# Optimization experiments

Hardware: AMD Instinct MI355X
Metric: run time of the kernel (lower is better)

## Reference

```python
import jax, jax.numpy as jnp
import numpy as np

BSZ, KW, D_MODEL, TEXT_DIM, VOCAB = 128, 8, 768, 512, 49408
EPS = 1e-8  # matches torch F.cosine_similarity eps


def setup_inputs() -> dict:
    key = jax.random.key(0)
    k1, k2, k3, k4 = jax.random.split(key, 4)
    return {
        "keywords": jax.random.normal(k1, (BSZ, KW, D_MODEL), dtype=jnp.float32),
        "W_proj": jax.random.normal(k2, (D_MODEL, TEXT_DIM), dtype=jnp.float32) * (1.0 / np.sqrt(D_MODEL)),
        "b_proj": jax.random.normal(k3, (TEXT_DIM,), dtype=jnp.float32) * 0.02,
        "W_emb": jax.random.normal(k4, (VOCAB, TEXT_DIM), dtype=jnp.float32) * 0.02,
    }


def reference(keywords, W_proj, b_proj, W_emb):
    # linear_proj: [B, K, d_model] -> [B, K, text_dim]
    kw = jnp.einsum("bkm,md->bkd", keywords, W_proj) + b_proj
    # cosine similarity of each keyword against the full token-embedding table
    kw_n = kw / jnp.maximum(jnp.linalg.norm(kw, axis=-1, keepdims=True), EPS)
    emb_n = W_emb / jnp.maximum(jnp.linalg.norm(W_emb, axis=-1, keepdims=True), EPS)
    cos_score = jnp.einsum("bkd,vd->bkv", kw_n, emb_n)  # [B, K, V]
    # soft VQ: subword probability over vocab
    subword_prob = jax.nn.softmax(cos_score, axis=-1)
    # soft assignment against the (frozen) embedding table
    kw_out = jnp.einsum("bkv,vd->bkd", subword_prob, W_emb)  # [B, K, text_dim]
    return kw_out, subword_prob, cos_score
```

## Files before the change

kernel.cpp:

```cpp
#include <hip/hip_runtime.h>

#define VOC 49408
#define TD 512
#define DM 768
#define NCOLG2 193
#define PV_S 32

typedef __attribute__((ext_vector_type(8))) short bf16x8;
typedef __attribute__((ext_vector_type(4))) short bf16x4;
typedef __attribute__((ext_vector_type(4))) float f32x4;

__device__ __forceinline__ unsigned short f2bf(float f) {
  unsigned int u = __float_as_uint(f);
  u += 0x7fffu + ((u >> 16) & 1u);
  return (unsigned short)(u >> 16);
}

__device__ __forceinline__ void gload16(const void* g, const void* l) {
  __builtin_amdgcn_global_load_lds(
      (const __attribute__((address_space(1))) void*)g,
      (__attribute__((address_space(3))) void*)l, 16, 0, 0);
}

__global__ __launch_bounds__(256) void k_proj(const float* __restrict__ kw,
                                              const float* __restrict__ Wp,
                                              const float* __restrict__ bp,
                                              unsigned short* __restrict__ kwn) {
  __shared__ float row_lds[4 * DM];
  __shared__ float rsum[4][4];
  __shared__ float rinv_s[4];
  const int t = threadIdx.x;
  const int rb = blockIdx.x * 4;
  for (int i = 0; i < 12; ++i) {
    int idx = i * 256 + t;
    row_lds[idx] = kw[(size_t)rb * DM + idx];
  }
  __syncthreads();
  float acc[4][2] = {};
  for (int m = 0; m < DM; ++m) {
    float w0 = Wp[m * TD + t];
    float w1 = Wp[m * TD + t + 256];
#pragma unroll
    for (int r = 0; r < 4; ++r) {
      float kv = row_lds[r * DM + m];
      acc[r][0] = fmaf(kv, w0, acc[r][0]);
      acc[r][1] = fmaf(kv, w1, acc[r][1]);
    }
  }
  const float b0 = bp[t], b1 = bp[t + 256];
  float p[4];
#pragma unroll
  for (int r = 0; r < 4; ++r) {
    acc[r][0] += b0;
    acc[r][1] += b1;
    p[r] = acc[r][0] * acc[r][0] + acc[r][1] * acc[r][1];
  }
#pragma unroll
  for (int off = 32; off; off >>= 1) {
#pragma unroll
    for (int r = 0; r < 4; ++r) p[r] += __shfl_down(p[r], off);
  }
  const int lane = t & 63, wv = t >> 6;
  if (lane == 0) {
#pragma unroll
    for (int r = 0; r < 4; ++r) rsum[r][wv] = p[r];
  }
  __syncthreads();
  if (t < 4) {
    float s = rsum[t][0] + rsum[t][1] + rsum[t][2] + rsum[t][3];
    rinv_s[t] = 1.0f / fmaxf(sqrtf(s), 1e-8f);
  }
  __syncthreads();
#pragma unroll
  for (int r = 0; r < 4; ++r) {
    float ri = rinv_s[r];
    kwn[(size_t)(rb + r) * TD + t] = f2bf(acc[r][0] * ri);
    kwn[(size_t)(rb + r) * TD + t + 256] = f2bf(acc[r][1] * ri);
  }
}

__global__ __launch_bounds__(256) void k_norms(const float* __restrict__ We,
                                               unsigned short* __restrict__ embB,
                                               float* __restrict__ rnormv) {
  const int t = threadIdx.x;
  const int lane = t & 63, w = t >> 6;
  const int v = blockIdx.x * 4 + w;
  const float* rowp = We + (size_t)v * TD;
  float4 a = *(const float4*)(rowp + lane * 8);
  float4 b = *(const float4*)(rowp + lane * 8 + 4);
  bf16x8 o;
  o[0] = (short)f2bf(a.x); o[1] = (short)f2bf(a.y);
  o[2] = (short)f2bf(a.z); o[3] = (short)f2bf(a.w);
  o[4] = (short)f2bf(b.x); o[5] = (short)f2bf(b.y);
  o[6] = (short)f2bf(b.z); o[7] = (short)f2bf(b.w);
  *(bf16x8*)(embB + (size_t)v * TD + lane * 8) = o;
  float ss = a.x * a.x + a.y * a.y + a.z * a.z + a.w * a.w +
             b.x * b.x + b.y * b.y + b.z * b.z + b.w * b.w;
#pragma unroll
  for (int off = 1; off < 64; off <<= 1) ss += __shfl_xor(ss, off);
  if (lane == 0) rnormv[v] = 1.0f / fmaxf(sqrtf(ss), 1e-8f);
}

__global__ __launch_bounds__(256) void k_transpose(const unsigned short* __restrict__ embB,
                                                   unsigned short* __restrict__ embT) {
  __shared__ unsigned short tile[64 * 72];
  const int t = threadIdx.x;
  const int d0 = blockIdx.x * 64, v0 = blockIdx.y * 64;
#pragma unroll
  for (int p = 0; p < 2; ++p) {
    int vl = p * 32 + (t >> 3), ch = t & 7;
    *(bf16x8*)&tile[vl * 72 + ch * 8] =
        *(const bf16x8*)(embB + (size_t)(v0 + vl) * TD + d0 + ch * 8);
  }
  __syncthreads();
#pragma unroll
  for (int p = 0; p < 2; ++p) {
    int dl = p * 32 + (t >> 3), vch = t & 7;
    bf16x8 o;
#pragma unroll
    for (int i = 0; i < 8; ++i) o[i] = (short)tile[(vch * 8 + i) * 72 + dl];
    *(bf16x8*)(embT + (size_t)(d0 + dl) * VOC + v0 + vch * 8) = o;
  }
}

__global__ __launch_bounds__(512, 2) void k_cos(const unsigned short* __restrict__ kwn,
                                                const unsigned short* __restrict__ embB,
                                                const float* __restrict__ rnormv,
                                                float* __restrict__ cosd,
                                                float* __restrict__ partial) {
  __shared__ unsigned short smem[2][2][256 * 64];
  const int t = threadIdx.x;
  const int lane = t & 63, w = t >> 6;
  const int wr = w & 3, wc = w >> 2;
  const int g = lane >> 4, l15 = lane & 15;
  const int rowg = blockIdx.x;
  const int colg = blockIdx.y;

  const int rl = lane >> 3;
  const int bsl = (lane & 7) ^ rl;

  f32x4 acc[4][8];
#pragma unroll
  for (int mi = 0; mi < 4; ++mi)
#pragma unroll
    for (int ni = 0; ni < 8; ++ni)
#pragma unroll
      for (int j = 0; j < 4; ++j) acc[mi][ni][j] = 0.0f;

  const unsigned short* Ag = kwn + (size_t)(rowg * 256 + w * 8 + rl) * TD + bsl * 8;
  const unsigned short* Bg = embB + (size_t)(colg * 256 + w * 8 + rl) * TD + bsl * 8;

#pragma unroll
  for (int i = 0; i < 4; ++i) {
    gload16(Ag + (size_t)(i * 64) * TD, (const void*)(&smem[0][0][(i * 64 + w * 8) * 64]));
    gload16(Bg + (size_t)(i * 64) * TD, (const void*)(&smem[0][1][(i * 64 + w * 8) * 64]));
  }
  __syncthreads();

  for (int kt = 0; kt < 8; ++kt) {
    const int buf = kt & 1;
    if (kt < 7) {
#pragma unroll
      for (int i = 0; i < 4; ++i) {
        gload16(Ag + (size_t)(i * 64) * TD + (kt + 1) * 64,
                (const void*)(&smem[buf ^ 1][0][(i * 64 + w * 8) * 64]));
        gload16(Bg + (size_t)(i * 64) * TD + (kt + 1) * 64,
                (const void*)(&smem[buf ^ 1][1][(i * 64 + w * 8) * 64]));
      }
    }
#pragma unroll
    for (int ks = 0; ks < 2; ++ks) {
      const int ch = (((ks * 4 + g) ^ (l15 & 7)) << 3);
      bf16x8 a[4];
#pragma unroll
      for (int mi = 0; mi < 4; ++mi)
        a[mi] = *(const bf16x8*)&smem[buf][0][(wr * 64 + mi * 16 + l15) * 64 + ch];
#pragma unroll
      for (int ni = 0; ni < 8; ++ni) {
        bf16x8 b = *(const bf16x8*)&smem[buf][1][(wc * 128 + ni * 16 + l15) * 64 + ch];
#pragma unroll
        for (int mi = 0; mi < 4; ++mi)
          acc[mi][ni] = __builtin_amdgcn_mfma_f32_16x16x32_bf16(a[mi], b, acc[mi][ni], 0, 0, 0);
      }
    }
    __syncthreads();
  }

  float (*rs)[256] = (float(*)[256]) & smem[0][0][0];
  const size_t rowbase = (size_t)rowg * 256 + wr * 64;
  const int colbase = colg * 256 + wc * 128;
  float rnv[8];
#pragma unroll
  for (int ni = 0; ni < 8; ++ni) rnv[ni] = rnormv[colbase + ni * 16 + l15];
#pragma unroll
  for (int mi = 0; mi < 4; ++mi) {
    float es[4] = {0.f, 0.f, 0.f, 0.f};
#pragma unroll
    for (int ni = 0; ni < 8; ++ni) {
#pragma unroll
      for (int j = 0; j < 4; ++j) {
        float c = acc[mi][ni][j] * rnv[ni];
        cosd[(rowbase + mi * 16 + g * 4 + j) * VOC + colbase + ni * 16 + l15] = c;
        es[j] += __expf(c);
      }
    }
#pragma unroll
    for (int j = 0; j < 4; ++j) {
      float e = es[j];
      e += __shfl_xor(e, 1);
      e += __shfl_xor(e, 2);
      e += __shfl_xor(e, 4);
      e += __shfl_xor(e, 8);
      if (l15 == 0) rs[wc][wr * 64 + mi * 16 + g * 4 + j] = e;
    }
  }
  __syncthreads();
  if (t < 256) {
    float srow = rs[0][t] + rs[1][t];
    partial[(size_t)colg * 1024 + rowg * 256 + t] = srow;
  }
}

__global__ __launch_bounds__(256) void k_denom(const float* __restrict__ partial,
                                               float* __restrict__ rdenom) {
  const int t = threadIdx.x;
  const int lane = t & 63, w = t >> 6;
  const int row = blockIdx.x * 4 + w;
  float s = 0.f;
  for (int c = lane; c < NCOLG2; c += 64) s += partial[(size_t)c * 1024 + row];
#pragma unroll
  for (int off = 1; off < 64; off <<= 1) s += __shfl_xor(s, off);
  if (lane == 0) rdenom[row] = 1.0f / s;
}

__global__ __launch_bounds__(512, 2) void k_pv(const float* __restrict__ cosd,
                                               const unsigned short* __restrict__ embT,
                                               const float* __restrict__ rdenom,
                                               float* __restrict__ prob,
                                               float* __restrict__ kpart) {
  __shared__ unsigned short smem[2][2][256 * 64];
  const int t = threadIdx.x;
  const int lane = t & 63, w = t >> 6;
  const int wr = w & 3, wc = w >> 2;
  const int g = lane >> 4, l15 = lane & 15;
  const int rowg = blockIdx.x;
  const int colg = blockIdx.y;
  const int s = blockIdx.z;
  const int t0 = s * 24 + (s < 4 ? s : 4);
  const int t1 = t0 + 24 + (s < 4 ? 1 : 0);

  const int ar = t >> 1, ah = t & 1;
  const int grow = rowg * 256 + ar;
  const float rdv = rdenom[grow];
  const float* cbase = cosd + (size_t)grow * VOC + ah * 4;
  float* pbase = prob + (size_t)grow * VOC + ah * 4;

  const int rl = lane >> 3;
  const int bsl = (lane & 7) ^ rl;

  f32x4 acc[4][8];
#pragma unroll
  for (int mi = 0; mi < 4; ++mi)
#pragma unroll
    for (int ni = 0; ni < 8; ++ni)
#pragma unroll
      for (int j = 0; j < 4; ++j) acc[mi][ni][j] = 0.0f;

  float4 cc[8];
  {
    const float* cp = cbase + (size_t)t0 * 64;
#pragma unroll
    for (int i = 0; i < 8; ++i) cc[i] = *(const float4*)(cp + i * 8);
  }

#pragma unroll
  for (int i = 0; i < 4; ++i) {
    gload16(embT + (size_t)(colg * 256 + i * 64 + w * 8 + rl) * VOC + t0 * 64 + bsl * 8,
            (const void*)(&smem[0][1][(i * 64 + w * 8) * 64]));
  }
  {
    const bool wp = (colg == (t0 & 1));
#pragma unroll
    for (int i = 0; i < 8; ++i) {
      float4 px;
      px.x = __expf(cc[i].x) * rdv;
      px.y = __expf(cc[i].y) * rdv;
      px.z = __expf(cc[i].z) * rdv;
      px.w = __expf(cc[i].w) * rdv;
      if (wp) *(float4*)(pbase + (size_t)t0 * 64 + i * 8) = px;
      bf16x4 b4;
      b4[0] = (short)f2bf(px.x);
      b4[1] = (short)f2bf(px.y);
      b4[2] = (short)f2bf(px.z);
      b4[3] = (short)f2bf(px.w);
      *(bf16x4*)&smem[0][0][ar * 64 + ((i ^ (ar & 7)) << 3) + ah * 4] = b4;
    }
  }
  if (t0 + 1 < t1) {
    const float* cp = cbase + (size_t)(t0 + 1) * 64;
#pragma unroll
    for (int i = 0; i < 8; ++i) cc[i] = *(const float4*)(cp + i * 8);
  }
  __syncthreads();

  for (int kt = t0; kt < t1; ++kt) {
    const int buf = (kt - t0) & 1;
    if (kt + 1 < t1) {
#pragma unroll
      for (int i = 0; i < 4; ++i) {
        gload16(embT + (size_t)(colg * 256 + i * 64 + w * 8 + rl) * VOC + (kt + 1) * 64 + bsl * 8,
                (const void*)(&smem[buf ^ 1][1][(i * 64 + w * 8) * 64]));
      }
      const bool wp = (colg == ((kt + 1) & 1));
#pragma unroll
      for (int i = 0; i < 8; ++i) {
        float4 px;
        px.x = __expf(cc[i].x) * rdv;
        px.y = __expf(cc[i].y) * rdv;
        px.z = __expf(cc[i].z) * rdv;
        px.w = __expf(cc[i].w) * rdv;
        if (wp) *(float4*)(pbase + (size_t)(kt + 1) * 64 + i * 8) = px;
        bf16x4 b4;
        b4[0] = (short)f2bf(px.x);
        b4[1] = (short)f2bf(px.y);
        b4[2] = (short)f2bf(px.z);
        b4[3] = (short)f2bf(px.w);
        *(bf16x4*)&smem[buf ^ 1][0][ar * 64 + ((i ^ (ar & 7)) << 3) + ah * 4] = b4;
      }
      if (kt + 2 < t1) {
        const float* cp = cbase + (size_t)(kt + 2) * 64;
#pragma unroll
        for (int i = 0; i < 8; ++i) cc[i] = *(const float4*)(cp + i * 8);
      }
    }
#pragma unroll
    for (int ks = 0; ks < 2; ++ks) {
      const int ch = (((ks * 4 + g) ^ (l15 & 7)) << 3);
      bf16x8 a[4];
#pragma unroll
      for (int mi = 0; mi < 4; ++mi)
        a[mi] = *(const bf16x8*)&smem[buf][0][(wr * 64 + mi * 16 + l15) * 64 + ch];
#pragma unroll
      for (int ni = 0; ni < 8; ++ni) {
        bf16x8 b = *(const bf16x8*)&smem[buf][1][(wc * 128 + ni * 16 + l15) * 64 + ch];
#pragma unroll
        for (int mi = 0; mi < 4; ++mi)
          acc[mi][ni] = __builtin_amdgcn_mfma_f32_16x16x32_bf16(a[mi], b, acc[mi][ni], 0, 0, 0);
      }
    }
    __syncthreads();
  }

#pragma unroll
  for (int mi = 0; mi < 4; ++mi)
#pragma unroll
    for (int ni = 0; ni < 8; ++ni)
#pragma unroll
      for (int j = 0; j < 4; ++j)
        kpart[((size_t)s * 1024 + rowg * 256 + wr * 64 + mi * 16 + g * 4 + j) * TD +
              colg * 256 + wc * 128 + ni * 16 + l15] = acc[mi][ni][j];
}

__global__ __launch_bounds__(256) void k_kwout(const float* __restrict__ kpart,
                                               float* __restrict__ outp) {
  const int gid = blockIdx.x * 256 + threadIdx.x;
  float4 s = {0.f, 0.f, 0.f, 0.f};
#pragma unroll
  for (int sp = 0; sp < PV_S; ++sp) {
    float4 v = *(const float4*)(kpart + (size_t)sp * 524288 + gid * 4);
    s.x += v.x; s.y += v.y; s.z += v.z; s.w += v.w;
  }
  *(float4*)(outp + gid * 4) = s;
}

extern "C" void kernel_launch(void* const* d_in, const int* in_sizes, int n_in,
                              void* d_out, int out_size, void* d_ws, size_t ws_size,
                              hipStream_t stream) {
  const float* kw = (const float*)d_in[0];
  const float* Wp = (const float*)d_in[1];
  const float* bp = (const float*)d_in[2];
  const float* We = (const float*)d_in[3];
  float* out = (float*)d_out;
  char* ws = (char*)d_ws;

  unsigned short* embT = (unsigned short*)ws;
  unsigned short* embB = (unsigned short*)(ws + 50593792);
  unsigned short* kwn = (unsigned short*)(ws + 101187584);
  float* rnormv = (float*)(ws + 102236160);
  float* partial = (float*)(ws + 102433792);
  float* rdenom = (float*)(ws + 103224320);
  float* kpart = (float*)(ws + 103228416);

  float* kwout = out;
  float* prob = out + 524288;
  float* cosd = out + 51118080;

  hipLaunchKernelGGL(k_proj, dim3(256), dim3(256), 0, stream, kw, Wp, bp, kwn);
  hipLaunchKernelGGL(k_norms, dim3(12352), dim3(256), 0, stream, We, embB, rnormv);
  hipLaunchKernelGGL(k_transpose, dim3(8, 772), dim3(256), 0, stream, embB, embT);
  hipLaunchKernelGGL(k_cos, dim3(4, NCOLG2), dim3(512), 0, stream, kwn, embB, rnormv,
                     cosd, partial);
  hipLaunchKernelGGL(k_denom, dim3(256), dim3(256), 0, stream, partial, rdenom);
  hipLaunchKernelGGL(k_pv, dim3(4, 2, PV_S), dim3(512), 0, stream, cosd, embT, rdenom,
                     prob, kpart);
  hipLaunchKernelGGL(k_kwout, dim3(512), dim3(256), 0, stream, kpart, kwout);
}
```

Before: 377.7 us.

## Store bf16 exp scores in cos kernel and feed them directly to PV

The cosine kernel now also writes exp(cos) as bf16 into a workspace buffer, staged through LDS for coalesced stores. The PV kernel loads that buffer with async global-to-LDS copies instead of rereading fp32 cos scores and recomputing exp. The 1/denominator scaling moves out of the MFMA operand into the final k_kwout reduction, and the prob output is written from the LDS tile. This halves the bytes read for the A operand and drops per-element exp work in PV, at the cost of an extra bf16 write of the full score matrix in k_cos and prob values rounded from bf16 exp.

Result: no change. 381.1 us (+0.9%).

```diff
diff --git a/kernel.cpp b/kernel.cpp
--- a/kernel.cpp
+++ b/kernel.cpp
@@ -14,6 +14,10 @@
   unsigned int u = __float_as_uint(f);
   u += 0x7fffu + ((u >> 16) & 1u);
   return (unsigned short)(u >> 16);
+}
+
+__device__ __forceinline__ float bf2f(unsigned short h) {
+  return __uint_as_float(((unsigned int)h) << 16);
 }
 
 __device__ __forceinline__ void gload16(const void* g, const void* l) {
@@ -127,8 +131,10 @@
                                                 const unsigned short* __restrict__ embB,
                                                 const float* __restrict__ rnormv,
                                                 float* __restrict__ cosd,
+                                                unsigned short* __restrict__ eb,
                                                 float* __restrict__ partial) {
   __shared__ unsigned short smem[2][2][256 * 64];
+  __shared__ float rs[2][256];
   const int t = threadIdx.x;
   const int lane = t & 63, w = t >> 6;
   const int wr = w & 3, wc = w >> 2;
@@ -186,7 +192,7 @@
     __syncthreads();
   }
 
-  float (*rs)[256] = (float(*)[256]) & smem[0][0][0];
+  unsigned short* els = &smem[0][0][0];
   const size_t rowbase = (size_t)rowg * 256 + wr * 64;
   const int colbase = colg * 256 + wc * 128;
   float rnv[8];
@@ -201,7 +207,9 @@
       for (int j = 0; j < 4; ++j) {
         float c = acc[mi][ni][j] * rnv[ni];
         cosd[(rowbase + mi * 16 + g * 4 + j) * VOC + colbase + ni * 16 + l15] = c;
-        es[j] += __expf(c);
+        float ev = __expf(c);
+        es[j] += ev;
+        els[(wr * 64 + mi * 16 + g * 4 + j) * 256 + wc * 128 + ni * 16 + l15] = f2bf(ev);
       }
     }
 #pragma unroll
@@ -215,6 +223,13 @@
     }
   }
   __syncthreads();
+#pragma unroll
+  for (int k = 0; k < 16; ++k) {
+    int id = k * 512 + t;
+    int r = id >> 5, c8 = id & 31;
+    *(bf16x8*)(eb + (size_t)(rowg * 256 + r) * VOC + colg * 256 + c8 * 8) =
+        *(const bf16x8*)&els[r * 256 + c8 * 8];
+  }
   if (t < 256) {
     float srow = rs[0][t] + rs[1][t];
     partial[(size_t)colg * 1024 + rowg * 256 + t] = srow;
@@ -233,7 +248,7 @@
   if (lane == 0) rdenom[row] = 1.0f / s;
 }
 
-__global__ __launch_bounds__(512, 2) void k_pv(const float* __restrict__ cosd,
+__global__ __launch_bounds__(512, 2) void k_pv(const unsigned short* __restrict__ eb,
                                                const unsigned short* __restrict__ embT,
                                                const float* __restrict__ rdenom,
                                                float* __restrict__ prob,
@@ -249,14 +264,13 @@
   const int t0 = s * 24 + (s < 4 ? s : 4);
   const int t1 = t0 + 24 + (s < 4 ? 1 : 0);
 
+  const int rl = lane >> 3;
+  const int bsl = (lane & 7) ^ rl;
+
   const int ar = t >> 1, ah = t & 1;
   const int grow = rowg * 256 + ar;
   const float rdv = rdenom[grow];
-  const float* cbase = cosd + (size_t)grow * VOC + ah * 4;
-  float* pbase = prob + (size_t)grow * VOC + ah * 4;
-
-  const int rl = lane >> 3;
-  const int bsl = (lane & 7) ^ rl;
+  float* pbase = prob + (size_t)grow * VOC;
 
   f32x4 acc[4][8];
 #pragma unroll
@@ -266,40 +280,13 @@
 #pragma unroll
       for (int j = 0; j < 4; ++j) acc[mi][ni][j] = 0.0f;
 
-  float4 cc[8];
-  {
-    const float* cp = cbase + (size_t)t0 * 64;
-#pragma unroll
-    for (int i = 0; i < 8; ++i) cc[i] = *(const float4*)(cp + i * 8);
-  }
+  const unsigned short* Ag = eb + (size_t)(rowg * 256 + w * 8 + rl) * VOC + bsl * 8;
+  const unsigned short* Bg = embT + (size_t)(colg * 256 + w * 8 + rl) * VOC + bsl * 8;
 
 #pragma unroll
   for (int i = 0; i < 4; ++i) {
-    gload16(embT + (size_t)(colg * 256 + i * 64 + w * 8 + rl) * VOC + t0 * 64 + bsl * 8,
-            (const void*)(&smem[0][1][(i * 64 + w * 8) * 64]));
-  }
-  {
-    const bool wp = (colg == (t0 & 1));
-#pragma unroll
-    for (int i = 0; i < 8; ++i) {
-      float4 px;
-      px.x = __expf(cc[i].x) * rdv;
-      px.y = __expf(cc[i].y) * rdv;
-      px.z = __expf(cc[i].z) * rdv;
-      px.w = __expf(cc[i].w) * rdv;
-      if (wp) *(float4*)(pbase + (size_t)t0 * 64 + i * 8) = px;
-      bf16x4 b4;
-      b4[0] = (short)f2bf(px.x);
-      b4[1] = (short)f2bf(px.y);
-      b4[2] = (short)f2bf(px.z);
-      b4[3] = (short)f2bf(px.w);
-      *(bf16x4*)&smem[0][0][ar * 64 + ((i ^ (ar & 7)) << 3) + ah * 4] = b4;
-    }
-  }
-  if (t0 + 1 < t1) {
-    const float* cp = cbase + (size_t)(t0 + 1) * 64;
-#pragma unroll
-    for (int i = 0; i < 8; ++i) cc[i] = *(const float4*)(cp + i * 8);
+    gload16(Ag + (size_t)(i * 64) * VOC + t0 * 64, (const void*)(&smem[0][0][(i * 64 + w * 8) * 64]));
+    gload16(Bg + (size_t)(i * 64) * VOC + t0 * 64, (const void*)(&smem[0][1][(i * 64 + w * 8) * 64]));
   }
   __syncthreads();
 
@@ -308,29 +295,10 @@
     if (kt + 1 < t1) {
 #pragma unroll
       for (int i = 0; i < 4; ++i) {
-        gload16(embT + (size_t)(colg * 256 + i * 64 + w * 8 + rl) * VOC + (kt + 1) * 64 + bsl * 8,
+        gload16(Ag + (size_t)(i * 64) * VOC + (kt + 1) * 64,
+                (const void*)(&smem[buf ^ 1][0][(i * 64 + w * 8) * 64]));
+        gload16(Bg + (size_t)(i * 64) * VOC + (kt + 1) * 64,
                 (const void*)(&smem[buf ^ 1][1][(i * 64 + w * 8) * 64]));
-      }
-      const bool wp = (colg == ((kt + 1) & 1));
-#pragma unroll
-      for (int i = 0; i < 8; ++i) {
-        float4 px;
-        px.x = __expf(cc[i].x) * rdv;
-        px.y = __expf(cc[i].y) * rdv;
-        px.z = __expf(cc[i].z) * rdv;
-        px.w = __expf(cc[i].w) * rdv;
-        if (wp) *(float4*)(pbase + (size_t)(kt + 1) * 64 + i * 8) = px;
-        bf16x4 b4;
-        b4[0] = (short)f2bf(px.x);
-        b4[1] = (short)f2bf(px.y);
-        b4[2] = (short)f2bf(px.z);
-        b4[3] = (short)f2bf(px.w);
-        *(bf16x4*)&smem[buf ^ 1][0][ar * 64 + ((i ^ (ar & 7)) << 3) + ah * 4] = b4;
-      }
-      if (kt + 2 < t1) {
-        const float* cp = cbase + (size_t)(kt + 2) * 64;
-#pragma unroll
-        for (int i = 0; i < 8; ++i) cc[i] = *(const float4*)(cp + i * 8);
       }
     }
 #pragma unroll
@@ -348,6 +316,24 @@
           acc[mi][ni] = __builtin_amdgcn_mfma_f32_16x16x32_bf16(a[mi], b, acc[mi][ni], 0, 0, 0);
       }
     }
+    if (colg == (kt & 1)) {
+#pragma unroll
+      for (int i = 0; i < 4; ++i) {
+        const int c8 = 2 * i + ah;
+        bf16x8 ev = *(const bf16x8*)&smem[buf][0][ar * 64 + ((c8 ^ (ar & 7)) << 3)];
+        float4 o0, o1;
+        o0.x = bf2f((unsigned short)ev[0]) * rdv;
+        o0.y = bf2f((unsigned short)ev[1]) * rdv;
+        o0.z = bf2f((unsigned short)ev[2]) * rdv;
+        o0.w = bf2f((unsigned short)ev[3]) * rdv;
+        o1.x = bf2f((unsigned short)ev[4]) * rdv;
+        o1.y = bf2f((unsigned short)ev[5]) * rdv;
+        o1.z = bf2f((unsigned short)ev[6]) * rdv;
+        o1.w = bf2f((unsigned short)ev[7]) * rdv;
+        *(float4*)(pbase + (size_t)kt * 64 + c8 * 8) = o0;
+        *(float4*)(pbase + (size_t)kt * 64 + c8 * 8 + 4) = o1;
+      }
+    }
     __syncthreads();
   }
 
@@ -362,15 +348,20 @@
 }
 
 __global__ __launch_bounds__(256) void k_kwout(const float* __restrict__ kpart,
+                                               const float* __restrict__ rdenom,
                                                float* __restrict__ outp) {
   const int gid = blockIdx.x * 256 + threadIdx.x;
+  const int row = gid >> 7;
   float4 s = {0.f, 0.f, 0.f, 0.f};
 #pragma unroll
   for (int sp = 0; sp < PV_S; ++sp) {
     float4 v = *(const float4*)(kpart + (size_t)sp * 524288 + gid * 4);
     s.x += v.x; s.y += v.y; s.z += v.z; s.w += v.w;
   }
-  *(float4*)(outp + gid * 4) = s;
+  const float rdv = rdenom[row];
+  float4 o;
+  o.x = s.x * rdv; o.y = s.y * rdv; o.z = s.z * rdv; o.w = s.w * rdv;
+  *(float4*)(outp + gid * 4) = o;
 }
 
 extern "C" void kernel_launch(void* const* d_in, const int* in_sizes, int n_in,
@@ -389,7 +380,8 @@
   float* rnormv = (float*)(ws + 102236160);
   float* partial = (float*)(ws + 102433792);
   float* rdenom = (float*)(ws + 103224320);
-  float* kpart = (float*)(ws + 103228416);
+  unsigned short* eb = (unsigned short*)(ws + 103228416);
+  float* kpart = (float*)(ws + 204416000);
 
   float* kwout = out;
   float* prob = out + 524288;
@@ -399,9 +391,9 @@
   hipLaunchKernelGGL(k_norms, dim3(12352), dim3(256), 0, stream, We, embB, rnormv);
   hipLaunchKernelGGL(k_transpose, dim3(8, 772), dim3(256), 0, stream, embB, embT);
   hipLaunchKernelGGL(k_cos, dim3(4, NCOLG2), dim3(512), 0, stream, kwn, embB, rnormv,
-                     cosd, partial);
+                     cosd, eb, partial);
   hipLaunchKernelGGL(k_denom, dim3(256), dim3(256), 0, stream, partial, rdenom);
-  hipLaunchKernelGGL(k_pv, dim3(4, 2, PV_S), dim3(512), 0, stream, cosd, embT, rdenom,
+  hipLaunchKernelGGL(k_pv, dim3(4, 2, PV_S), dim3(512), 0, stream, eb, embT, rdenom,
                      prob, kpart);
-  hipLaunchKernelGGL(k_kwout, dim3(512), dim3(256), 0, stream, kpart, kwout);
-}
+  hipLaunchKernelGGL(k_kwout, dim3(512), dim3(256), 0, stream, kpart, rdenom, kwout);
+}
```

## Retile PV kernel to full-width 128x512 tiles so softmax is computed once

Applied to the files above, without the earlier changes.

The PV kernel used 256x256 output tiles split over two column groups, so every cosine score was read and exponentiated twice, once per column group. It now uses 128-row by 512-column tiles with K-steps of 32, so each block covers the full text dimension and every prob element is computed and stored exactly once. This halves the cosd reads and the exp work, at the cost of smaller K steps with more barriers per unit of work and reloading embT once per row group. The k_cos row-sum scratch is also moved into its own shared array instead of aliasing the tile buffer.

Result: slower. 408.9 us (+8.2%).

```diff
diff --git a/kernel.cpp b/kernel.cpp
--- a/kernel.cpp
+++ b/kernel.cpp
@@ -129,6 +129,7 @@
                                                 float* __restrict__ cosd,
                                                 float* __restrict__ partial) {
   __shared__ unsigned short smem[2][2][256 * 64];
+  __shared__ float rs[2][256];
   const int t = threadIdx.x;
   const int lane = t & 63, w = t >> 6;
   const int wr = w & 3, wc = w >> 2;
@@ -186,7 +187,6 @@
     __syncthreads();
   }
 
-  float (*rs)[256] = (float(*)[256]) & smem[0][0][0];
   const size_t rowbase = (size_t)rowg * 256 + wr * 64;
   const int colbase = colg * 256 + wc * 128;
   float rnv[8];
@@ -238,25 +238,26 @@
                                                const float* __restrict__ rdenom,
                                                float* __restrict__ prob,
                                                float* __restrict__ kpart) {
-  __shared__ unsigned short smem[2][2][256 * 64];
+  __shared__ unsigned short As[2][128 * 32];
+  __shared__ unsigned short Bs[2][512 * 32];
   const int t = threadIdx.x;
   const int lane = t & 63, w = t >> 6;
-  const int wr = w & 3, wc = w >> 2;
+  const int wr = w & 1, wc = w >> 1;
   const int g = lane >> 4, l15 = lane & 15;
   const int rowg = blockIdx.x;
-  const int colg = blockIdx.y;
-  const int s = blockIdx.z;
-  const int t0 = s * 24 + (s < 4 ? s : 4);
-  const int t1 = t0 + 24 + (s < 4 ? 1 : 0);
-
-  const int ar = t >> 1, ah = t & 1;
-  const int grow = rowg * 256 + ar;
+  const int s = blockIdx.y;
+  const int t0 = s * 48 + (s < 8 ? s : 8);
+  const int t1 = t0 + 48 + (s < 8 ? 1 : 0);
+
+  const int ar = t >> 2, q = t & 3;
+  const int grow = rowg * 128 + ar;
   const float rdv = rdenom[grow];
-  const float* cbase = cosd + (size_t)grow * VOC + ah * 4;
-  float* pbase = prob + (size_t)grow * VOC + ah * 4;
-
-  const int rl = lane >> 3;
-  const int bsl = (lane & 7) ^ rl;
+  const float* cbase = cosd + (size_t)grow * VOC + q * 8;
+  float* pbase = prob + (size_t)grow * VOC + q * 8;
+  const int aoff = ar * 32 + ((q ^ (ar & 3)) << 3);
+
+  const int rl4 = lane >> 2;
+  const int bsl = (lane & 3) ^ (rl4 & 3);
 
   f32x4 acc[4][8];
 #pragma unroll
@@ -266,40 +267,37 @@
 #pragma unroll
       for (int j = 0; j < 4; ++j) acc[mi][ni][j] = 0.0f;
 
-  float4 cc[8];
+  float4 c0, c1;
   {
-    const float* cp = cbase + (size_t)t0 * 64;
-#pragma unroll
-    for (int i = 0; i < 8; ++i) cc[i] = *(const float4*)(cp + i * 8);
+    const float* cp = cbase + (size_t)t0 * 32;
+    c0 = *(const float4*)cp;
+    c1 = *(const float4*)(cp + 4);
   }
 
 #pragma unroll
   for (int i = 0; i < 4; ++i) {
-    gload16(embT + (size_t)(colg * 256 + i * 64 + w * 8 + rl) * VOC + t0 * 64 + bsl * 8,
-            (const void*)(&smem[0][1][(i * 64 + w * 8) * 64]));
+    gload16(embT + (size_t)(w * 64 + i * 16 + rl4) * VOC + t0 * 32 + bsl * 8,
+            (const void*)(&Bs[0][(w * 64 + i * 16) * 32]));
   }
   {
-    const bool wp = (colg == (t0 & 1));
-#pragma unroll
-    for (int i = 0; i < 8; ++i) {
-      float4 px;
-      px.x = __expf(cc[i].x) * rdv;
-      px.y = __expf(cc[i].y) * rdv;
-      px.z = __expf(cc[i].z) * rdv;
-      px.w = __expf(cc[i].w) * rdv;
-      if (wp) *(float4*)(pbase + (size_t)t0 * 64 + i * 8) = px;
-      bf16x4 b4;
-      b4[0] = (short)f2bf(px.x);
-      b4[1] = (short)f2bf(px.y);
-      b4[2] = (short)f2bf(px.z);
-      b4[3] = (short)f2bf(px.w);
-      *(bf16x4*)&smem[0][0][ar * 64 + ((i ^ (ar & 7)) << 3) + ah * 4] = b4;
-    }
+    float4 p0, p1;
+    p0.x = __expf(c0.x) * rdv; p0.y = __expf(c0.y) * rdv;
+    p0.z = __expf(c0.z) * rdv; p0.w = __expf(c0.w) * rdv;
+    p1.x = __expf(c1.x) * rdv; p1.y = __expf(c1.y) * rdv;
+    p1.z = __expf(c1.z) * rdv; p1.w = __expf(c1.w) * rdv;
+    *(float4*)(pbase + (size_t)t0 * 32) = p0;
+    *(float4*)(pbase + (size_t)t0 * 32 + 4) = p1;
+    bf16x8 a8;
+    a8[0] = (short)f2bf(p0.x); a8[1] = (short)f2bf(p0.y);
+    a8[2] = (short)f2bf(p0.z); a8[3] = (short)f2bf(p0.w);
+    a8[4] = (short)f2bf(p1.x); a8[5] = (short)f2bf(p1.y);
+    a8[6] = (short)f2bf(p1.z); a8[7] = (short)f2bf(p1.w);
+    *(bf16x8*)&As[0][aoff] = a8;
   }
   if (t0 + 1 < t1) {
-    const float* cp = cbase + (size_t)(t0 + 1) * 64;
-#pragma unroll
-    for (int i = 0; i < 8; ++i) cc[i] = *(const float4*)(cp + i * 8);
+    const float* cp = cbase + (size_t)(t0 + 1) * 32;
+    c0 = *(const float4*)cp;
+    c1 = *(const float4*)(cp + 4);
   }
   __syncthreads();
 
@@ -308,41 +306,37 @@
     if (kt + 1 < t1) {
 #pragma unroll
       for (int i = 0; i < 4; ++i) {
-        gload16(embT + (size_t)(colg * 256 + i * 64 + w * 8 + rl) * VOC + (kt + 1) * 64 + bsl * 8,
-                (const void*)(&smem[buf ^ 1][1][(i * 64 + w * 8) * 64]));
-      }
-      const bool wp = (colg == ((kt + 1) & 1));
-#pragma unroll
-      for (int i = 0; i < 8; ++i) {
-        float4 px;
-        px.x = __expf(cc[i].x) * rdv;
-        px.y = __expf(cc[i].y) * rdv;
-        px.z = __expf(cc[i].z) * rdv;
-        px.w = __expf(cc[i].w) * rdv;
-        if (wp) *(float4*)(pbase + (size_t)(kt + 1) * 64 + i * 8) = px;
-        bf16x4 b4;
-        b4[0] = (short)f2bf(px.x);
-        b4[1] = (short)f2bf(px.y);
-        b4[2] = (short)f2bf(px.z);
-        b4[3] = (short)f2bf(px.w);
-        *(bf16x4*)&smem[buf ^ 1][0][ar * 64 + ((i ^ (ar & 7)) << 3) + ah * 4] = b4;
-      }
+        gload16(embT + (size_t)(w * 64 + i * 16 + rl4) * VOC + (kt + 1) * 32 + bsl * 8,
+                (const void*)(&Bs[buf ^ 1][(w * 64 + i * 16) * 32]));
+      }
+      float4 p0, p1;
+      p0.x = __expf(c0.x) * rdv; p0.y = __expf(c0.y) * rdv;
+      p0.z = __expf(c0.z) * rdv; p0.w = __expf(c0.w) * rdv;
+      p1.x = __expf(c1.x) * rdv; p1.y = __expf(c1.y) * rdv;
+      p1.z = __expf(c1.z) * rdv; p1.w = __expf(c1.w) * rdv;
+      *(float4*)(pbase + (size_t)(kt + 1) * 32) = p0;
+      *(float4*)(pbase + (size_t)(kt + 1) * 32 + 4) = p1;
+      bf16x8 a8;
+      a8[0] = (short)f2bf(p0.x); a8[1] = (short)f2bf(p0.y);
+      a8[2] = (short)f2bf(p0.z); a8[3] = (short)f2bf(p0.w);
+      a8[4] = (short)f2bf(p1.x); a8[5] = (short)f2bf(p1.y);
+      a8[6] = (short)f2bf(p1.z); a8[7] = (short)f2bf(p1.w);
+      *(bf16x8*)&As[buf ^ 1][aoff] = a8;
       if (kt + 2 < t1) {
-        const float* cp = cbase + (size_t)(kt + 2) * 64;
-#pragma unroll
-        for (int i = 0; i < 8; ++i) cc[i] = *(const float4*)(cp + i * 8);
-      }
-    }
-#pragma unroll
-    for (int ks = 0; ks < 2; ++ks) {
-      const int ch = (((ks * 4 + g) ^ (l15 & 7)) << 3);
+        const float* cp = cbase + (size_t)(kt + 2) * 32;
+        c0 = *(const float4*)cp;
+        c1 = *(const float4*)(cp + 4);
+      }
+    }
+    {
+      const int ch = ((g ^ (l15 & 3)) << 3);
       bf16x8 a[4];
 #pragma unroll
       for (int mi = 0; mi < 4; ++mi)
-        a[mi] = *(const bf16x8*)&smem[buf][0][(wr * 64 + mi * 16 + l15) * 64 + ch];
+        a[mi] = *(const bf16x8*)&As[buf][(wr * 64 + mi * 16 + l15) * 32 + ch];
 #pragma unroll
       for (int ni = 0; ni < 8; ++ni) {
-        bf16x8 b = *(const bf16x8*)&smem[buf][1][(wc * 128 + ni * 16 + l15) * 64 + ch];
+        bf16x8 b = *(const bf16x8*)&Bs[buf][(wc * 128 + ni * 16 + l15) * 32 + ch];
 #pragma unroll
         for (int mi = 0; mi < 4; ++mi)
           acc[mi][ni] = __builtin_amdgcn_mfma_f32_16x16x32_bf16(a[mi], b, acc[mi][ni], 0, 0, 0);
@@ -357,8 +351,8 @@
     for (int ni = 0; ni < 8; ++ni)
 #pragma unroll
       for (int j = 0; j < 4; ++j)
-        kpart[((size_t)s * 1024 + rowg * 256 + wr * 64 + mi * 16 + g * 4 + j) * TD +
-              colg * 256 + wc * 128 + ni * 16 + l15] = acc[mi][ni][j];
+        kpart[((size_t)s * 1024 + rowg * 128 + wr * 64 + mi * 16 + g * 4 + j) * TD +
+              wc * 128 + ni * 16 + l15] = acc[mi][ni][j];
 }
 
 __global__ __launch_bounds__(256) void k_kwout(const float* __restrict__ kpart,
@@ -401,7 +395,7 @@
   hipLaunchKernelGGL(k_cos, dim3(4, NCOLG2), dim3(512), 0, stream, kwn, embB, rnormv,
                      cosd, partial);
   hipLaunchKernelGGL(k_denom, dim3(256), dim3(256), 0, stream, partial, rdenom);
-  hipLaunchKernelGGL(k_pv, dim3(4, 2, PV_S), dim3(512), 0, stream, cosd, embT, rdenom,
+  hipLaunchKernelGGL(k_pv, dim3(8, PV_S), dim3(512), 0, stream, cosd, embT, rdenom,
                      prob, kpart);
   hipLaunchKernelGGL(k_kwout, dim3(512), dim3(256), 0, stream, kpart, kwout);
 }
```
